# Kernel tuning notes

Hardware: AMD Instinct MI355X
Metric: run time of the kernel (lower is better)

Reference implementation:

```python
import jax, jax.numpy as jnp
import numpy as np

ALPHA = 0.9
BETA = 0.85
THRESHOLD = 0.1
SURR_SCALE = 100.0  # SpyTorch-style surrogate gradient scale


@jax.custom_vjp
def surr_spike(x):
    # Heaviside forward, surrogate gradient backward (SurrGradSpike)
    return (x > 0.0).astype(x.dtype)


def _surr_fwd(x):
    return surr_spike(x), x


def _surr_bwd(x, g):
    return (g / (SURR_SCALE * jnp.abs(x) + 1.0) ** 2,)


surr_spike.defvjp(_surr_fwd, _surr_bwd)


def setup_inputs() -> dict:
    key = jax.random.key(0)
    k1, k2, k3 = jax.random.split(key, 3)
    B, T, D_IN, N = 64, 256, 512, 1024
    inputs = jax.random.normal(k1, (B, T, D_IN), dtype=jnp.float32)
    weights = 0.1 * jax.random.normal(k2, (D_IN, N), dtype=jnp.float32)
    recurrent_weights = 0.1 * jax.random.normal(k3, (N, N), dtype=jnp.float32)
    return {"inputs": inputs, "weights": weights, "recurrent_weights": recurrent_weights}


def reference(inputs, weights, recurrent_weights):
    B, T, D_IN = inputs.shape
    N = weights.shape[1]

    def step(carry, x_t):
        mem, syn, spk = carry
        h = jnp.einsum('bd,dn->bn', x_t, weights)          # input projection
        rec_h = jnp.einsum('bn,nm->bm', spk, recurrent_weights)  # recurrent drive
        new_syn = ALPHA * syn + h + rec_h
        new_mem = BETA * mem + new_syn
        mthr = new_mem - THRESHOLD
        out = surr_spike(mthr)
        new_mem = jnp.where(mthr > 0.0, jnp.zeros_like(new_mem), new_mem)  # reset
        return (new_mem, new_syn, out), (out, new_mem, new_syn)

    zeros = jnp.zeros((B, N), dtype=inputs.dtype)
    init = (zeros, zeros, zeros)
    x_tbd = jnp.transpose(inputs, (1, 0, 2))  # [T, B, D]
    (mem, syn, spk), (spk_rec, mem_rec, syn_rec) = jax.lax.scan(step, init, x_tbd)
    # back to [B, T, N]
    spk_rec = jnp.transpose(spk_rec, (1, 0, 2))
    mem_rec = jnp.transpose(mem_rec, (1, 0, 2))
    syn_rec = jnp.transpose(syn_rec, (1, 0, 2))
    return (spk_rec, (mem, syn, spk), (mem_rec, syn_rec))
```

## Files before the change

kernel.cpp:

```cpp
#include <hip/hip_runtime.h>

typedef __attribute__((ext_vector_type(8))) _Float16 f16x8;
typedef __attribute__((ext_vector_type(4))) float f32x4;

static constexpr int   B_  = 64;
static constexpr int   T_  = 256;
static constexpr int   D_  = 512;
static constexpr int   N_  = 1024;
static constexpr float ALPHA_ = 0.9f;
static constexpr float BETA_  = 0.85f;
static constexpr float THR_   = 0.1f;

__global__ __launch_bounds__(256) void dsrnn_hgemm(const float* __restrict__ X,
                                                   const float* __restrict__ W,
                                                   float* __restrict__ H) {
  __shared__ float As[16][128];
  __shared__ float Bs[16][128];
  const int tid = threadIdx.x;
  const int nb  = blockIdx.x & 7;
  const int mb  = blockIdx.x >> 3;
  const int r0  = mb << 7;
  const int n0  = nb << 7;

  float acc[8][8];
#pragma unroll
  for (int i = 0; i < 8; ++i)
#pragma unroll
    for (int j = 0; j < 8; ++j) acc[i][j] = 0.f;

  for (int k0 = 0; k0 < D_; k0 += 16) {
#pragma unroll
    for (int i = 0; i < 2; ++i) {
      const int f   = tid * 2 + i;
      const int row = f >> 2;
      const int kq  = (f & 3) << 2;
      const float4 v =
          *reinterpret_cast<const float4*>(&X[(size_t)(r0 + row) * D_ + k0 + kq]);
      As[kq + 0][row] = v.x;
      As[kq + 1][row] = v.y;
      As[kq + 2][row] = v.z;
      As[kq + 3][row] = v.w;
    }
#pragma unroll
    for (int i = 0; i < 2; ++i) {
      const int f  = tid * 2 + i;
      const int kr = f >> 5;
      const int c  = (f & 31) << 2;
      *reinterpret_cast<float4*>(&Bs[kr][c]) =
          *reinterpret_cast<const float4*>(&W[(size_t)(k0 + kr) * N_ + n0 + c]);
    }
    __syncthreads();
    const int ty = tid >> 4, tx = tid & 15;
#pragma unroll
    for (int kk = 0; kk < 16; ++kk) {
      float a[8], b[8];
      *reinterpret_cast<float4*>(&a[0]) = *reinterpret_cast<const float4*>(&As[kk][ty * 8]);
      *reinterpret_cast<float4*>(&a[4]) = *reinterpret_cast<const float4*>(&As[kk][ty * 8 + 4]);
      *reinterpret_cast<float4*>(&b[0]) = *reinterpret_cast<const float4*>(&Bs[kk][tx * 8]);
      *reinterpret_cast<float4*>(&b[4]) = *reinterpret_cast<const float4*>(&Bs[kk][tx * 8 + 4]);
#pragma unroll
      for (int i = 0; i < 8; ++i)
#pragma unroll
        for (int j = 0; j < 8; ++j) acc[i][j] = fmaf(a[i], b[j], acc[i][j]);
    }
    __syncthreads();
  }
  const int ty = tid >> 4, tx = tid & 15;
#pragma unroll
  for (int i = 0; i < 8; ++i) {
    const size_t r = (size_t)(r0 + ty * 8 + i);
#pragma unroll
    for (int j = 0; j < 8; j += 4)
      *reinterpret_cast<float4*>(&H[r * N_ + n0 + tx * 8 + j]) =
          *reinterpret_cast<const float4*>(&acc[i][j]);
  }
}

__global__ __launch_bounds__(256, 1) void dsrnn_step9(
    const float* __restrict__ Rw,
    float* __restrict__ spk_rec,
    float* __restrict__ mem_rec,
    float* __restrict__ syn_rec,
    float* __restrict__ mem_fin,
    float* __restrict__ syn_fin,
    float* __restrict__ spk_fin,
    unsigned long long* masks)
{
  extern __shared__ unsigned char RsB[];
  __shared__ unsigned smaskU[16][33];
  __shared__ float scratch[4][512];

  const int tid  = threadIdx.x;
  const int bq   = blockIdx.x >> 5;
  const int mg   = blockIdx.x & 31;
  const int wv   = tid >> 6;
  const int lane = tid & 63;
  const int kg   = lane >> 4;
  const int cc   = lane & 15;

  for (int k = 0; k < 128; ++k) {
    const int e  = (k << 8) + tid;
    const int n  = e >> 5;
    const int ml = e & 31;
    const float v = Rw[(size_t)n * N_ + (mg << 5) + ml];
    const _Float16 hi = (_Float16)v;
    const float hif = (float)hi;
    const _Float16 lo = (_Float16)((v - hif) * 4096.0f);
    const int s   = n >> 5;
    const int kin = n & 31;
    const int ln  = ((kin >> 3) << 4) + (ml & 15);
    const int mt  = ml >> 4;
    const int off = ((((s << 1) + mt) << 1) << 10) + (ln << 4) + ((kin & 7) << 1);
    *(_Float16*)(RsB + off)        = hi;
    *(_Float16*)(RsB + off + 1024) = lo;
  }

  const int bl1 = tid >> 5;
  const int bl2 = bl1 + 8;
  const int ml_ = tid & 31;
  const int b1  = (bq << 4) + bl1;
  const int b2  = (bq << 4) + bl2;
  const int m   = (mg << 5) + ml_;

  float mem1 = 0.f, syn1 = 0.f, spv1 = 0.f;
  float mem2 = 0.f, syn2 = 0.f, spv2 = 0.f;

  __syncthreads();

  for (int t = 0; t < T_; ++t) {
    const size_t i1 = ((size_t)b1 * T_ + t) * N_ + m;
    const size_t i2 = ((size_t)b2 * T_ + t) * N_ + m;
    const float h1 = syn_rec[i1];
    const float h2 = syn_rec[i2];

    {
      unsigned long long* base = masks + (size_t)(t & 1) * 2048;
      unsigned long long* p1 = base + (size_t)b1 * 32 + ml_;
      unsigned long long* p2 = base + (size_t)b2 * 32 + ml_;
      unsigned long long w1 =
          __hip_atomic_load(p1, __ATOMIC_RELAXED, __HIP_MEMORY_SCOPE_AGENT);
      unsigned long long w2 =
          __hip_atomic_load(p2, __ATOMIC_RELAXED, __HIP_MEMORY_SCOPE_AGENT);
      int g = 0;
      while ((((unsigned)(w1 >> 32) != (unsigned)t) |
              ((unsigned)(w2 >> 32) != (unsigned)t)) && ++g < (1 << 20)) {
        __builtin_amdgcn_s_sleep(1);
        w1 = __hip_atomic_load(p1, __ATOMIC_RELAXED, __HIP_MEMORY_SCOPE_AGENT);
        w2 = __hip_atomic_load(p2, __ATOMIC_RELAXED, __HIP_MEMORY_SCOPE_AGENT);
      }
      smaskU[bl1][ml_] = (unsigned)w1;
      smaskU[bl2][ml_] = (unsigned)w2;
    }
    __syncthreads();

    f32x4 c0h = {0.f, 0.f, 0.f, 0.f};
    f32x4 c0l = {0.f, 0.f, 0.f, 0.f};
    f32x4 c1h = {0.f, 0.f, 0.f, 0.f};
    f32x4 c1l = {0.f, 0.f, 0.f, 0.f};
    const int shB = kg << 3;
#pragma unroll
    for (int ss = 0; ss < 8; ++ss) {
      const int s = (wv << 3) + ss;
      const unsigned bits8 = (smaskU[cc][s] >> shB) & 0xFFu;
      union { unsigned u[4]; f16x8 v; } A;
#pragma unroll
      for (int p = 0; p < 4; ++p) {
        const unsigned e0 = (bits8 >> (2 * p)) & 1u;
        const unsigned e1 = (bits8 >> (2 * p + 1)) & 1u;
        A.u[p] = e0 * 0x3C00u + e1 * 0x3C000000u;
      }
      const unsigned char* sb = RsB + (s << 12) + (lane << 4);
      const f16x8 b00 = *reinterpret_cast<const f16x8*>(sb);
      const f16x8 b01 = *reinterpret_cast<const f16x8*>(sb + 1024);
      const f16x8 b10 = *reinterpret_cast<const f16x8*>(sb + 2048);
      const f16x8 b11 = *reinterpret_cast<const f16x8*>(sb + 3072);
      c0h = __builtin_amdgcn_mfma_f32_16x16x32_f16(A.v, b00, c0h, 0, 0, 0);
      c0l = __builtin_amdgcn_mfma_f32_16x16x32_f16(A.v, b01, c0l, 0, 0, 0);
      c1h = __builtin_amdgcn_mfma_f32_16x16x32_f16(A.v, b10, c1h, 0, 0, 0);
      c1l = __builtin_amdgcn_mfma_f32_16x16x32_f16(A.v, b11, c1l, 0, 0, 0);
    }
    constexpr float INV4096 = 1.0f / 4096.0f;
#pragma unroll
    for (int r = 0; r < 4; ++r) {
      const int row = (kg << 2) + r;
      scratch[wv][(row << 5) + cc]      = fmaf(c0l[r], INV4096, c0h[r]);
      scratch[wv][(row << 5) + cc + 16] = fmaf(c1l[r], INV4096, c1h[r]);
    }
    __syncthreads();

    const int o1 = (bl1 << 5) + ml_;
    const int o2 = (bl2 << 5) + ml_;
    const float rec1 =
        scratch[0][o1] + scratch[1][o1] + scratch[2][o1] + scratch[3][o1];
    const float rec2 =
        scratch[0][o2] + scratch[1][o2] + scratch[2][o2] + scratch[3][o2];

    syn1 = ALPHA_ * syn1 + h1 + rec1;
    mem1 = BETA_ * mem1 + syn1;
    const bool sp1 = (mem1 - THR_) > 0.f;
    spv1 = sp1 ? 1.f : 0.f;
    mem1 = sp1 ? 0.f : mem1;

    syn2 = ALPHA_ * syn2 + h2 + rec2;
    mem2 = BETA_ * mem2 + syn2;
    const bool sp2 = (mem2 - THR_) > 0.f;
    spv2 = sp2 ? 1.f : 0.f;
    mem2 = sp2 ? 0.f : mem2;

    const unsigned long long ball1 = __ballot(sp1);
    const unsigned long long ball2 = __ballot(sp2);
    if (ml_ == 0) {
      const unsigned sh = lane & 32;
      const unsigned long long tag = ((unsigned long long)(unsigned)(t + 1)) << 32;
      unsigned long long* nb = masks + (size_t)((t + 1) & 1) * 2048;
      __hip_atomic_store(nb + (size_t)b1 * 32 + mg,
                         tag | (unsigned)(ball1 >> sh),
                         __ATOMIC_RELAXED, __HIP_MEMORY_SCOPE_AGENT);
      __hip_atomic_store(nb + (size_t)b2 * 32 + mg,
                         tag | (unsigned)(ball2 >> sh),
                         __ATOMIC_RELAXED, __HIP_MEMORY_SCOPE_AGENT);
    }

    spk_rec[i1] = spv1; mem_rec[i1] = mem1; syn_rec[i1] = syn1;
    spk_rec[i2] = spv2; mem_rec[i2] = mem2; syn_rec[i2] = syn2;
  }

  mem_fin[b1 * N_ + m] = mem1; syn_fin[b1 * N_ + m] = syn1; spk_fin[b1 * N_ + m] = spv1;
  mem_fin[b2 * N_ + m] = mem2; syn_fin[b2 * N_ + m] = syn2; spk_fin[b2 * N_ + m] = spv2;
}

extern "C" void kernel_launch(void* const* d_in, const int* in_sizes, int n_in,
                              void* d_out, int out_size, void* d_ws, size_t ws_size,
                              hipStream_t stream) {
  const float* X  = (const float*)d_in[0];
  const float* W  = (const float*)d_in[1];
  const float* Rw = (const float*)d_in[2];

  float* out = (float*)d_out;
  const size_t BTN = (size_t)B_ * T_ * N_;
  const size_t BN  = (size_t)B_ * N_;
  float* spk_rec = out;
  float* mem_fin = out + BTN;
  float* syn_fin = mem_fin + BN;
  float* spk_fin = syn_fin + BN;
  float* mem_rec = spk_fin + BN;
  float* syn_rec = mem_rec + BTN;

  unsigned long long* masks = (unsigned long long*)d_ws;
  hipMemsetAsync(d_ws, 0, (size_t)2 * 64 * 32 * sizeof(unsigned long long), stream);

  dsrnn_hgemm<<<dim3(1024), dim3(256), 0, stream>>>(X, W, syn_rec);

  (void)hipFuncSetAttribute((const void*)dsrnn_step9,
                            hipFuncAttributeMaxDynamicSharedMemorySize, 131072);
  void* args[] = {(void*)&Rw,      (void*)&spk_rec, (void*)&mem_rec,
                  (void*)&syn_rec, (void*)&mem_fin, (void*)&syn_fin,
                  (void*)&spk_fin, (void*)&masks};
  hipLaunchCooperativeKernel((void*)dsrnn_step9, dim3(128), dim3(256), args,
                             131072, stream);
}
```

Measured before the change: 866.3 us.

## Move input projection to split-fp16 MFMA and defer per-step record stores

Replaces the fp32 FMA GEMM for the input projection with an MFMA GEMM. Both operands are split into fp16 hi and scaled-lo parts, and W is pre-packed into fragment layout by a new kernel that writes into the not-yet-used mem_rec output buffer. In the recurrent kernel, each step's spk/mem/syn record stores are held in registers and issued during the next step's mask wait, to overlap global stores with synchronisation latency. The three-MFMA split drops the lo*lo term, which slightly reduces precision, and reusing the output buffer as scratch depends on the later kernel overwriting it.

```diff
diff --git a/kernel.cpp b/kernel.cpp
--- a/kernel.cpp
+++ b/kernel.cpp
@@ -10,73 +10,113 @@
 static constexpr float ALPHA_ = 0.9f;
 static constexpr float BETA_  = 0.85f;
 static constexpr float THR_   = 0.1f;
-
-__global__ __launch_bounds__(256) void dsrnn_hgemm(const float* __restrict__ X,
-                                                   const float* __restrict__ W,
-                                                   float* __restrict__ H) {
-  __shared__ float As[16][128];
-  __shared__ float Bs[16][128];
-  const int tid = threadIdx.x;
-  const int nb  = blockIdx.x & 7;
-  const int mb  = blockIdx.x >> 3;
-  const int r0  = mb << 7;
-  const int n0  = nb << 7;
-
-  float acc[8][8];
-#pragma unroll
-  for (int i = 0; i < 8; ++i)
-#pragma unroll
-    for (int j = 0; j < 8; ++j) acc[i][j] = 0.f;
-
-  for (int k0 = 0; k0 < D_; k0 += 16) {
-#pragma unroll
-    for (int i = 0; i < 2; ++i) {
-      const int f   = tid * 2 + i;
-      const int row = f >> 2;
-      const int kq  = (f & 3) << 2;
-      const float4 v =
-          *reinterpret_cast<const float4*>(&X[(size_t)(r0 + row) * D_ + k0 + kq]);
-      As[kq + 0][row] = v.x;
-      As[kq + 1][row] = v.y;
-      As[kq + 2][row] = v.z;
-      As[kq + 3][row] = v.w;
-    }
-#pragma unroll
-    for (int i = 0; i < 2; ++i) {
-      const int f  = tid * 2 + i;
-      const int kr = f >> 5;
-      const int c  = (f & 31) << 2;
-      *reinterpret_cast<float4*>(&Bs[kr][c]) =
-          *reinterpret_cast<const float4*>(&W[(size_t)(k0 + kr) * N_ + n0 + c]);
+static constexpr float INV4096 = 1.0f / 4096.0f;
+
+__global__ __launch_bounds__(256) void dsrnn_wsplit(const float* __restrict__ W,
+                                                    unsigned char* __restrict__ Wfrag) {
+  const int u    = blockIdx.x * 256 + threadIdx.x;
+  const int lane = u & 63;
+  const int bi   = u >> 6;
+  const int cf   = bi >> 4;
+  const int chk  = bi & 15;
+  const int kg   = lane >> 4;
+  const int cc   = lane & 15;
+  const int n    = cf * 16 + cc;
+  const int k0   = chk * 32 + kg * 8;
+  f16x8 vh, vl;
+#pragma unroll
+  for (int j = 0; j < 8; ++j) {
+    const float v = W[(size_t)(k0 + j) * N_ + n];
+    const _Float16 h = (_Float16)v;
+    vh[j] = h;
+    vl[j] = (_Float16)((v - (float)h) * 4096.0f);
+  }
+  unsigned char* dst = Wfrag + (size_t)bi * 2048 + lane * 16;
+  *reinterpret_cast<f16x8*>(dst)        = vh;
+  *reinterpret_cast<f16x8*>(dst + 1024) = vl;
+}
+
+__global__ __launch_bounds__(256) void dsrnn_hgemm2(const float* __restrict__ X,
+                                                    const unsigned char* __restrict__ Wfrag,
+                                                    float* __restrict__ H) {
+  __shared__ __align__(16) _Float16 Xa_hi[64][40];
+  __shared__ __align__(16) _Float16 Xa_lo[64][40];
+  const int tid  = threadIdx.x;
+  const int rb   = blockIdx.x >> 3;
+  const int nb   = (blockIdx.x & 7) << 7;
+  const int r0   = rb << 6;
+  const int wv   = tid >> 6;
+  const int lane = tid & 63;
+  const int kg   = lane >> 4;
+  const int cc   = lane & 15;
+
+  f32x4 ah[4][2], am[4][2];
+#pragma unroll
+  for (int i = 0; i < 4; ++i)
+#pragma unroll
+    for (int j = 0; j < 2; ++j) {
+      ah[i][j] = (f32x4){0.f, 0.f, 0.f, 0.f};
+      am[i][j] = (f32x4){0.f, 0.f, 0.f, 0.f};
+    }
+
+  const int srow = tid >> 2;
+  const int skq  = (tid & 3) << 3;
+
+  for (int kc = 0; kc < 16; ++kc) {
+    {
+      const float* xp = X + (size_t)(r0 + srow) * D_ + kc * 32 + skq;
+      const float4 v0 = *reinterpret_cast<const float4*>(xp);
+      const float4 v1 = *reinterpret_cast<const float4*>(xp + 4);
+      const float vv[8] = {v0.x, v0.y, v0.z, v0.w, v1.x, v1.y, v1.z, v1.w};
+      f16x8 xh, xl;
+#pragma unroll
+      for (int j = 0; j < 8; ++j) {
+        const _Float16 h = (_Float16)vv[j];
+        xh[j] = h;
+        xl[j] = (_Float16)((vv[j] - (float)h) * 4096.0f);
+      }
+      *reinterpret_cast<f16x8*>(&Xa_hi[srow][skq]) = xh;
+      *reinterpret_cast<f16x8*>(&Xa_lo[srow][skq]) = xl;
     }
     __syncthreads();
-    const int ty = tid >> 4, tx = tid & 15;
-#pragma unroll
-    for (int kk = 0; kk < 16; ++kk) {
-      float a[8], b[8];
-      *reinterpret_cast<float4*>(&a[0]) = *reinterpret_cast<const float4*>(&As[kk][ty * 8]);
-      *reinterpret_cast<float4*>(&a[4]) = *reinterpret_cast<const float4*>(&As[kk][ty * 8 + 4]);
-      *reinterpret_cast<float4*>(&b[0]) = *reinterpret_cast<const float4*>(&Bs[kk][tx * 8]);
-      *reinterpret_cast<float4*>(&b[4]) = *reinterpret_cast<const float4*>(&Bs[kk][tx * 8 + 4]);
-#pragma unroll
-      for (int i = 0; i < 8; ++i)
-#pragma unroll
-        for (int j = 0; j < 8; ++j) acc[i][j] = fmaf(a[i], b[j], acc[i][j]);
+
+    f16x8 Bh[2], Bl[2];
+#pragma unroll
+    for (int cfi = 0; cfi < 2; ++cfi) {
+      const unsigned char* bp =
+          Wfrag + (size_t)((((nb >> 4) + (wv << 1) + cfi) * 16 + kc) * 2048) + lane * 16;
+      Bh[cfi] = *reinterpret_cast<const f16x8*>(bp);
+      Bl[cfi] = *reinterpret_cast<const f16x8*>(bp + 1024);
+    }
+
+#pragma unroll
+    for (int rf = 0; rf < 4; ++rf) {
+      const f16x8 Ah = *reinterpret_cast<const f16x8*>(&Xa_hi[rf * 16 + cc][kg * 8]);
+      const f16x8 Al = *reinterpret_cast<const f16x8*>(&Xa_lo[rf * 16 + cc][kg * 8]);
+#pragma unroll
+      for (int cfi = 0; cfi < 2; ++cfi) {
+        ah[rf][cfi] = __builtin_amdgcn_mfma_f32_16x16x32_f16(Ah, Bh[cfi], ah[rf][cfi], 0, 0, 0);
+        am[rf][cfi] = __builtin_amdgcn_mfma_f32_16x16x32_f16(Ah, Bl[cfi], am[rf][cfi], 0, 0, 0);
+        am[rf][cfi] = __builtin_amdgcn_mfma_f32_16x16x32_f16(Al, Bh[cfi], am[rf][cfi], 0, 0, 0);
+      }
     }
     __syncthreads();
   }
-  const int ty = tid >> 4, tx = tid & 15;
-#pragma unroll
-  for (int i = 0; i < 8; ++i) {
-    const size_t r = (size_t)(r0 + ty * 8 + i);
-#pragma unroll
-    for (int j = 0; j < 8; j += 4)
-      *reinterpret_cast<float4*>(&H[r * N_ + n0 + tx * 8 + j]) =
-          *reinterpret_cast<const float4*>(&acc[i][j]);
-  }
+
+#pragma unroll
+  for (int rf = 0; rf < 4; ++rf)
+#pragma unroll
+    for (int cfi = 0; cfi < 2; ++cfi) {
+      const int col = nb + wv * 32 + cfi * 16 + cc;
+#pragma unroll
+      for (int rr = 0; rr < 4; ++rr) {
+        const int row = r0 + rf * 16 + kg * 4 + rr;
+        H[(size_t)row * N_ + col] = fmaf(am[rf][cfi][rr], INV4096, ah[rf][cfi][rr]);
+      }
+    }
 }
 
-__global__ __launch_bounds__(256, 1) void dsrnn_step9(
+__global__ __launch_bounds__(256, 1) void dsrnn_step10(
     const float* __restrict__ Rw,
     float* __restrict__ spk_rec,
     float* __restrict__ mem_rec,
@@ -124,6 +164,8 @@
 
   float mem1 = 0.f, syn1 = 0.f, spv1 = 0.f;
   float mem2 = 0.f, syn2 = 0.f, spv2 = 0.f;
+  float po1s = 0.f, po1m = 0.f, po1y = 0.f;
+  float po2s = 0.f, po2m = 0.f, po2y = 0.f;
 
   __syncthreads();
 
@@ -151,6 +193,11 @@
       smaskU[bl1][ml_] = (unsigned)w1;
       smaskU[bl2][ml_] = (unsigned)w2;
     }
+
+    if (t > 0) {
+      spk_rec[i1 - N_] = po1s; mem_rec[i1 - N_] = po1m; syn_rec[i1 - N_] = po1y;
+      spk_rec[i2 - N_] = po2s; mem_rec[i2 - N_] = po2m; syn_rec[i2 - N_] = po2y;
+    }
     __syncthreads();
 
     f32x4 c0h = {0.f, 0.f, 0.f, 0.f};
@@ -179,7 +226,6 @@
       c1h = __builtin_amdgcn_mfma_f32_16x16x32_f16(A.v, b10, c1h, 0, 0, 0);
       c1l = __builtin_amdgcn_mfma_f32_16x16x32_f16(A.v, b11, c1l, 0, 0, 0);
     }
-    constexpr float INV4096 = 1.0f / 4096.0f;
 #pragma unroll
     for (int r = 0; r < 4; ++r) {
       const int row = (kg << 2) + r;
@@ -221,10 +267,14 @@
                          __ATOMIC_RELAXED, __HIP_MEMORY_SCOPE_AGENT);
     }
 
-    spk_rec[i1] = spv1; mem_rec[i1] = mem1; syn_rec[i1] = syn1;
-    spk_rec[i2] = spv2; mem_rec[i2] = mem2; syn_rec[i2] = syn2;
+    po1s = spv1; po1m = mem1; po1y = syn1;
+    po2s = spv2; po2m = mem2; po2y = syn2;
   }
 
+  const size_t l1 = ((size_t)b1 * T_ + (T_ - 1)) * N_ + m;
+  const size_t l2 = ((size_t)b2 * T_ + (T_ - 1)) * N_ + m;
+  spk_rec[l1] = po1s; mem_rec[l1] = po1m; syn_rec[l1] = po1y;
+  spk_rec[l2] = po2s; mem_rec[l2] = po2m; syn_rec[l2] = po2y;
   mem_fin[b1 * N_ + m] = mem1; syn_fin[b1 * N_ + m] = syn1; spk_fin[b1 * N_ + m] = spv1;
   mem_fin[b2 * N_ + m] = mem2; syn_fin[b2 * N_ + m] = syn2; spk_fin[b2 * N_ + m] = spv2;
 }
@@ -246,16 +296,19 @@
   float* mem_rec = spk_fin + BN;
   float* syn_rec = mem_rec + BTN;
 
+  unsigned char* Wfrag = (unsigned char*)mem_rec;
+
   unsigned long long* masks = (unsigned long long*)d_ws;
   hipMemsetAsync(d_ws, 0, (size_t)2 * 64 * 32 * sizeof(unsigned long long), stream);
 
-  dsrnn_hgemm<<<dim3(1024), dim3(256), 0, stream>>>(X, W, syn_rec);
-
-  (void)hipFuncSetAttribute((const void*)dsrnn_step9,
+  dsrnn_wsplit<<<dim3(256), dim3(256), 0, stream>>>(W, Wfrag);
+  dsrnn_hgemm2<<<dim3(2048), dim3(256), 0, stream>>>(X, Wfrag, syn_rec);
+
+  (void)hipFuncSetAttribute((const void*)dsrnn_step10,
                             hipFuncAttributeMaxDynamicSharedMemorySize, 131072);
   void* args[] = {(void*)&Rw,      (void*)&spk_rec, (void*)&mem_rec,
                   (void*)&syn_rec, (void*)&mem_fin, (void*)&syn_fin,
                   (void*)&spk_fin, (void*)&masks};
-  hipLaunchCooperativeKernel((void*)dsrnn_step9, dim3(128), dim3(256), args,
+  hipLaunchCooperativeKernel((void*)dsrnn_step10, dim3(128), dim3(256), args,
                              131072, stream);
 }
```

Result: faster. 769.8 us (-11.1%).

## Fuse input projection into recurrent kernel with split-fp16 MFMA, prefetched a step ahead

Applied to the files above, without the earlier changes.

Removes the separate FP32 SIMT GEMM that wrote the input projection into syn_rec. The recurrent cooperative kernel now keeps its slice of W in registers as hi/lo fp16 pairs. It computes each step's projection with MFMA (three products for near-fp32 accuracy) one timestep ahead, and loads X rows two steps ahead. This drops the standalone GEMM launch and the write-then-read of a 64MB buffer, and lets the projection overlap the spin-wait on spike masks. The cost is extra MFMA work and register pressure inside the latency-bound sequential loop.

```diff
diff --git a/kernel.cpp b/kernel.cpp
--- a/kernel.cpp
+++ b/kernel.cpp
@@ -10,74 +10,12 @@
 static constexpr float ALPHA_ = 0.9f;
 static constexpr float BETA_  = 0.85f;
 static constexpr float THR_   = 0.1f;
-
-__global__ __launch_bounds__(256) void dsrnn_hgemm(const float* __restrict__ X,
-                                                   const float* __restrict__ W,
-                                                   float* __restrict__ H) {
-  __shared__ float As[16][128];
-  __shared__ float Bs[16][128];
-  const int tid = threadIdx.x;
-  const int nb  = blockIdx.x & 7;
-  const int mb  = blockIdx.x >> 3;
-  const int r0  = mb << 7;
-  const int n0  = nb << 7;
-
-  float acc[8][8];
-#pragma unroll
-  for (int i = 0; i < 8; ++i)
-#pragma unroll
-    for (int j = 0; j < 8; ++j) acc[i][j] = 0.f;
-
-  for (int k0 = 0; k0 < D_; k0 += 16) {
-#pragma unroll
-    for (int i = 0; i < 2; ++i) {
-      const int f   = tid * 2 + i;
-      const int row = f >> 2;
-      const int kq  = (f & 3) << 2;
-      const float4 v =
-          *reinterpret_cast<const float4*>(&X[(size_t)(r0 + row) * D_ + k0 + kq]);
-      As[kq + 0][row] = v.x;
-      As[kq + 1][row] = v.y;
-      As[kq + 2][row] = v.z;
-      As[kq + 3][row] = v.w;
-    }
-#pragma unroll
-    for (int i = 0; i < 2; ++i) {
-      const int f  = tid * 2 + i;
-      const int kr = f >> 5;
-      const int c  = (f & 31) << 2;
-      *reinterpret_cast<float4*>(&Bs[kr][c]) =
-          *reinterpret_cast<const float4*>(&W[(size_t)(k0 + kr) * N_ + n0 + c]);
-    }
-    __syncthreads();
-    const int ty = tid >> 4, tx = tid & 15;
-#pragma unroll
-    for (int kk = 0; kk < 16; ++kk) {
-      float a[8], b[8];
-      *reinterpret_cast<float4*>(&a[0]) = *reinterpret_cast<const float4*>(&As[kk][ty * 8]);
-      *reinterpret_cast<float4*>(&a[4]) = *reinterpret_cast<const float4*>(&As[kk][ty * 8 + 4]);
-      *reinterpret_cast<float4*>(&b[0]) = *reinterpret_cast<const float4*>(&Bs[kk][tx * 8]);
-      *reinterpret_cast<float4*>(&b[4]) = *reinterpret_cast<const float4*>(&Bs[kk][tx * 8 + 4]);
-#pragma unroll
-      for (int i = 0; i < 8; ++i)
-#pragma unroll
-        for (int j = 0; j < 8; ++j) acc[i][j] = fmaf(a[i], b[j], acc[i][j]);
-    }
-    __syncthreads();
-  }
-  const int ty = tid >> 4, tx = tid & 15;
-#pragma unroll
-  for (int i = 0; i < 8; ++i) {
-    const size_t r = (size_t)(r0 + ty * 8 + i);
-#pragma unroll
-    for (int j = 0; j < 8; j += 4)
-      *reinterpret_cast<float4*>(&H[r * N_ + n0 + tx * 8 + j]) =
-          *reinterpret_cast<const float4*>(&acc[i][j]);
-  }
-}
-
-__global__ __launch_bounds__(256, 1) void dsrnn_step9(
+static constexpr float INV4096 = 1.0f / 4096.0f;
+
+__global__ __launch_bounds__(256, 1) void dsrnn_step15(
     const float* __restrict__ Rw,
+    const float* __restrict__ Wg,
+    const float* __restrict__ Xg,
     float* __restrict__ spk_rec,
     float* __restrict__ mem_rec,
     float* __restrict__ syn_rec,
@@ -89,6 +27,7 @@
   extern __shared__ unsigned char RsB[];
   __shared__ unsigned smaskU[16][33];
   __shared__ float scratch[4][512];
+  __shared__ float hscr[2][4][512];
 
   const int tid  = threadIdx.x;
   const int bq   = blockIdx.x >> 5;
@@ -115,23 +54,102 @@
     *(_Float16*)(RsB + off + 1024) = lo;
   }
 
+  f16x8 whi[4][2], wlo[4][2];
+#pragma unroll
+  for (int kci = 0; kci < 4; ++kci)
+#pragma unroll
+    for (int mt = 0; mt < 2; ++mt) {
+      const float* wp = Wg + (size_t)((wv << 7) + (kci << 5) + (kg << 3)) * N_
+                        + (mg << 5) + (mt << 4) + cc;
+#pragma unroll
+      for (int j = 0; j < 8; ++j) {
+        const float v = wp[(size_t)j * N_];
+        const _Float16 h = (_Float16)v;
+        whi[kci][mt][j] = h;
+        wlo[kci][mt][j] = (_Float16)((v - (float)h) * 4096.0f);
+      }
+    }
+
   const int bl1 = tid >> 5;
   const int bl2 = bl1 + 8;
   const int ml_ = tid & 31;
   const int b1  = (bq << 4) + bl1;
   const int b2  = (bq << 4) + bl2;
   const int m   = (mg << 5) + ml_;
+  const int o1  = (bl1 << 5) + ml_;
+  const int o2  = (bl2 << 5) + ml_;
+
+#define LOADX(TT)                                                           \
+  {                                                                         \
+    const float* xp = Xg + ((size_t)((bq << 4) + cc) * T_ + (TT)) * D_      \
+                      + (wv << 7) + (kg << 3);                              \
+    _Pragma("unroll")                                                       \
+    for (int kci = 0; kci < 4; ++kci) {                                     \
+      xr[kci][0] = *reinterpret_cast<const float4*>(xp + (kci << 5));       \
+      xr[kci][1] = *reinterpret_cast<const float4*>(xp + (kci << 5) + 4);   \
+    }                                                                       \
+  }
+
+#define HCOMP(HPTR)                                                         \
+  {                                                                         \
+    f32x4 hh0 = {0.f,0.f,0.f,0.f}, hh1 = {0.f,0.f,0.f,0.f};                 \
+    f32x4 hm0 = {0.f,0.f,0.f,0.f}, hm1 = {0.f,0.f,0.f,0.f};                 \
+    _Pragma("unroll")                                                       \
+    for (int kci = 0; kci < 4; ++kci) {                                     \
+      f16x8 Ah, Al;                                                         \
+      const float* xf0 = (const float*)&xr[kci][0];                         \
+      const float* xf1 = (const float*)&xr[kci][1];                         \
+      _Pragma("unroll")                                                     \
+      for (int j = 0; j < 4; ++j) {                                         \
+        float v = xf0[j];                                                   \
+        _Float16 hq = (_Float16)v;                                          \
+        Ah[j] = hq; Al[j] = (_Float16)((v - (float)hq) * 4096.0f);          \
+        v = xf1[j];                                                         \
+        hq = (_Float16)v;                                                   \
+        Ah[j + 4] = hq; Al[j + 4] = (_Float16)((v - (float)hq) * 4096.0f);  \
+      }                                                                     \
+      hh0 = __builtin_amdgcn_mfma_f32_16x16x32_f16(Ah, whi[kci][0], hh0, 0, 0, 0); \
+      hm0 = __builtin_amdgcn_mfma_f32_16x16x32_f16(Ah, wlo[kci][0], hm0, 0, 0, 0); \
+      hm0 = __builtin_amdgcn_mfma_f32_16x16x32_f16(Al, whi[kci][0], hm0, 0, 0, 0); \
+      hh1 = __builtin_amdgcn_mfma_f32_16x16x32_f16(Ah, whi[kci][1], hh1, 0, 0, 0); \
+      hm1 = __builtin_amdgcn_mfma_f32_16x16x32_f16(Ah, wlo[kci][1], hm1, 0, 0, 0); \
+      hm1 = __builtin_amdgcn_mfma_f32_16x16x32_f16(Al, whi[kci][1], hm1, 0, 0, 0); \
+    }                                                                       \
+    _Pragma("unroll")                                                       \
+    for (int r = 0; r < 4; ++r) {                                           \
+      const int row = (kg << 2) + r;                                        \
+      (HPTR)[(row << 5) + cc]      = fmaf(hm0[r], INV4096, hh0[r]);         \
+      (HPTR)[(row << 5) + cc + 16] = fmaf(hm1[r], INV4096, hh1[r]);         \
+    }                                                                       \
+  }
 
   float mem1 = 0.f, syn1 = 0.f, spv1 = 0.f;
   float mem2 = 0.f, syn2 = 0.f, spv2 = 0.f;
+  float4 xr[4][2];
 
   __syncthreads();
+
+  LOADX(0);
+  HCOMP(&hscr[0][wv][0]);
+  __syncthreads();
+  float h1, h2;
+  {
+    const float* hc = &hscr[0][0][0];
+    h1 = hc[o1] + hc[512 + o1] + hc[1024 + o1] + hc[1536 + o1];
+    h2 = hc[o2] + hc[512 + o2] + hc[1024 + o2] + hc[1536 + o2];
+  }
+  LOADX(1);
 
   for (int t = 0; t < T_; ++t) {
     const size_t i1 = ((size_t)b1 * T_ + t) * N_ + m;
     const size_t i2 = ((size_t)b2 * T_ + t) * N_ + m;
-    const float h1 = syn_rec[i1];
-    const float h2 = syn_rec[i2];
+
+    HCOMP(&hscr[(t + 1) & 1][wv][0]);
+
+    {
+      const int tn = (t + 2 < T_) ? (t + 2) : (T_ - 1);
+      LOADX(tn);
+    }
 
     {
       unsigned long long* base = masks + (size_t)(t & 1) * 2048;
@@ -179,7 +197,6 @@
       c1h = __builtin_amdgcn_mfma_f32_16x16x32_f16(A.v, b10, c1h, 0, 0, 0);
       c1l = __builtin_amdgcn_mfma_f32_16x16x32_f16(A.v, b11, c1l, 0, 0, 0);
     }
-    constexpr float INV4096 = 1.0f / 4096.0f;
 #pragma unroll
     for (int r = 0; r < 4; ++r) {
       const int row = (kg << 2) + r;
@@ -188,12 +205,13 @@
     }
     __syncthreads();
 
-    const int o1 = (bl1 << 5) + ml_;
-    const int o2 = (bl2 << 5) + ml_;
     const float rec1 =
         scratch[0][o1] + scratch[1][o1] + scratch[2][o1] + scratch[3][o1];
     const float rec2 =
         scratch[0][o2] + scratch[1][o2] + scratch[2][o2] + scratch[3][o2];
+    const float* hc = &hscr[(t + 1) & 1][0][0];
+    const float hn1 = hc[o1] + hc[512 + o1] + hc[1024 + o1] + hc[1536 + o1];
+    const float hn2 = hc[o2] + hc[512 + o2] + hc[1024 + o2] + hc[1536 + o2];
 
     syn1 = ALPHA_ * syn1 + h1 + rec1;
     mem1 = BETA_ * mem1 + syn1;
@@ -223,10 +241,14 @@
 
     spk_rec[i1] = spv1; mem_rec[i1] = mem1; syn_rec[i1] = syn1;
     spk_rec[i2] = spv2; mem_rec[i2] = mem2; syn_rec[i2] = syn2;
+
+    h1 = hn1; h2 = hn2;
   }
 
   mem_fin[b1 * N_ + m] = mem1; syn_fin[b1 * N_ + m] = syn1; spk_fin[b1 * N_ + m] = spv1;
   mem_fin[b2 * N_ + m] = mem2; syn_fin[b2 * N_ + m] = syn2; spk_fin[b2 * N_ + m] = spv2;
+#undef LOADX
+#undef HCOMP
 }
 
 extern "C" void kernel_launch(void* const* d_in, const int* in_sizes, int n_in,
@@ -247,15 +269,14 @@
   float* syn_rec = mem_rec + BTN;
 
   unsigned long long* masks = (unsigned long long*)d_ws;
-  hipMemsetAsync(d_ws, 0, (size_t)2 * 64 * 32 * sizeof(unsigned long long), stream);
-
-  dsrnn_hgemm<<<dim3(1024), dim3(256), 0, stream>>>(X, W, syn_rec);
-
-  (void)hipFuncSetAttribute((const void*)dsrnn_step9,
+  hipMemsetAsync(d_ws, 0, (size_t)2 * 2048 * sizeof(unsigned long long), stream);
+
+  (void)hipFuncSetAttribute((const void*)dsrnn_step15,
                             hipFuncAttributeMaxDynamicSharedMemorySize, 131072);
-  void* args[] = {(void*)&Rw,      (void*)&spk_rec, (void*)&mem_rec,
-                  (void*)&syn_rec, (void*)&mem_fin, (void*)&syn_fin,
-                  (void*)&spk_fin, (void*)&masks};
-  hipLaunchCooperativeKernel((void*)dsrnn_step9, dim3(128), dim3(256), args,
+  void* args[] = {(void*)&Rw,      (void*)&W,       (void*)&X,
+                  (void*)&spk_rec, (void*)&mem_rec, (void*)&syn_rec,
+                  (void*)&mem_fin, (void*)&syn_fin, (void*)&spk_fin,
+                  (void*)&masks};
+  hipLaunchCooperativeKernel((void*)dsrnn_step15, dim3(128), dim3(256), args,
                              131072, stream);
 }
```

Result: no change. 863.9 us (-0.3%).
